# Optimization experiments

Hardware: AMD Instinct MI355X
Metric: run time of the kernel (lower is better)

Reference implementation:

```python
import jax, jax.numpy as jnp
import numpy as np

T, H, I, E, K = 16384, 2048, 1024, 8, 2  # tokens, hidden, intermediate, experts, top_k


def setup_inputs() -> dict:
    key = jax.random.key(0)
    k1, k2, k3, k4, k5 = jax.random.split(key, 5)
    hidden_states = jax.random.normal(k1, (T, H), dtype=jnp.float32)
    expert_routing_table = jax.random.randint(k2, (T, K), 0, E, dtype=jnp.int32)
    rw = jax.random.uniform(k3, (T, K), dtype=jnp.float32)
    router_weights = rw  # op consumes raw per-token gate weights
    # fused gate+up projection per expert: [E, 2I, H] (Linear-style [out, in])
    w13 = jax.random.normal(k4, (E, 2 * I, H), dtype=jnp.float32) * (1.0 / np.sqrt(H))
    # down projection per expert: [E, H, I]
    w2 = jax.random.normal(k5, (E, H, I), dtype=jnp.float32) * (1.0 / np.sqrt(I))
    return {
        "hidden_states": hidden_states,
        "expert_routing_table": expert_routing_table,
        "router_weights": router_weights,
        "w13": w13,
        "w2": w2,
    }


def reference(hidden_states, expert_routing_table, router_weights, w13, w2):
    # Faithful math of torch.ops.hpu.mixture_of_experts (silu activation):
    # for each token t and each routed expert e (top-k):
    #   g, u = split(x_t @ w13_e^T); y += router_w * ((silu(g) * u) @ w2_e^T)
    num_experts = w13.shape[0]
    out = jnp.zeros_like(hidden_states)
    for e in range(num_experts):  # small fixed expert loop
        # combine weight for expert e per token: sum over top-k slots routed to e
        coef = jnp.sum(
            jnp.where(expert_routing_table == e, router_weights, 0.0), axis=-1
        )  # [T]
        gu = hidden_states @ w13[e].T            # [T, 2I]
        g, u = jnp.split(gu, 2, axis=-1)         # SwiGLU halves
        act = jax.nn.silu(g) * u                 # [T, I]
        out = out + coef[:, None] * (act @ w2[e].T)  # [T, H]
    return out
```

## Files before the change

kernel.cpp:

```cpp
#include <hip/hip_runtime.h>
#include <hip/hip_bf16.h>
#include <stdint.h>

#define TOKS 16384
#define HDIM 2048
#define IDIM 1024
#define NEXP 8
#define TOPK 2
#define NPAIR (TOKS*TOPK)

typedef __attribute__((ext_vector_type(4))) float f32x4;
typedef __attribute__((ext_vector_type(8))) __bf16 bf16x8;
typedef __attribute__((ext_vector_type(8))) unsigned short u16x8;

#define GLOAD_LDS16(gp, lp) \
  __builtin_amdgcn_global_load_lds((const __attribute__((address_space(1))) void*)(gp), \
                                   (__attribute__((address_space(3))) void*)(lp), 16, 0, 0)

#define LGKM_WAITN(n) asm volatile("s_waitcnt lgkmcnt(" #n ")" ::: "memory")
#define VM_WAITN(n)   asm volatile("s_waitcnt vmcnt(" #n ")" ::: "memory")

__device__ __forceinline__ unsigned short f2bf(float f) {
  unsigned int u = __float_as_uint(f);
  u += 0x7FFF + ((u >> 16) & 1);
  return (unsigned short)(u >> 16);
}
__device__ __forceinline__ float bf2f(unsigned short h) {
  return __uint_as_float(((unsigned int)h) << 16);
}

#define W13_N8 (NEXP * 2 * IDIM * HDIM / 8)
#define W2_N8  (NEXP * HDIM * IDIM / 8)
#define X_N8   (TOKS * HDIM / 8)
__global__ __launch_bounds__(256) void cvt_all(const float* __restrict__ w13,
                                               const float* __restrict__ w2,
                                               const float* __restrict__ x,
                                               unsigned short* __restrict__ w13b,
                                               unsigned short* __restrict__ w2b,
                                               unsigned short* __restrict__ xb) {
  int i = blockIdx.x * 256 + threadIdx.x;
  const float* s; unsigned short* d; int j;
  if (i < W13_N8)              { s = w13; d = w13b; j = i; }
  else if (i < W13_N8 + W2_N8) { s = w2;  d = w2b;  j = i - W13_N8; }
  else                         { s = x;   d = xb;   j = i - W13_N8 - W2_N8; }
  const float4* sp = (const float4*)s + (size_t)j * 2;
  float4 a = sp[0], b = sp[1];
  u16x8 o;
  o[0] = f2bf(a.x); o[1] = f2bf(a.y); o[2] = f2bf(a.z); o[3] = f2bf(a.w);
  o[4] = f2bf(b.x); o[5] = f2bf(b.y); o[6] = f2bf(b.z); o[7] = f2bf(b.w);
  *((u16x8*)d + j) = o;
}

__global__ void route_count(const int* __restrict__ ert, int* __restrict__ ctrl) {
  int p = blockIdx.x * 256 + threadIdx.x;
  if (p < NPAIR) atomicAdd(&ctrl[ert[p]], 1);
}

__global__ void route_scan(int* __restrict__ ctrl) {
  if (blockIdx.x == 0 && threadIdx.x == 0) {
    int off = 0;
    for (int e = 0; e < NEXP; ++e) { ctrl[8 + e] = off; ctrl[16 + e] = off; off += ctrl[e]; }
    int toff = 0;
    for (int e = 0; e < NEXP; ++e) { ctrl[24 + e] = toff; toff += (ctrl[e] + 255) >> 8; }
    ctrl[32] = toff;
  }
}

__global__ void route_scatter(const int* __restrict__ ert, const float* __restrict__ rw,
                              int* __restrict__ ctrl, int* __restrict__ porig,
                              float* __restrict__ pcoef, int* __restrict__ pinv) {
  int p = blockIdx.x * 256 + threadIdx.x;
  if (p < NPAIR) {
    int e = ert[p];
    int pos = atomicAdd(&ctrl[16 + e], 1);
    porig[pos] = p;
    pcoef[pos] = rw[p];
    pinv[p]    = pos;
  }
}


#define RD_SET(lb, A0v, A1v, B0v, B1v) do {                                          \
  _Pragma("unroll") for (int mi = 0; mi < 4; ++mi) {                                 \
    int r_ = wr * 128 + mi * 16 + l15;                                               \
    A0v[mi] = *(const bf16x8*)((lb) + r_ * 64 + ((l16 ^ ((r_ >> 1) & 3)) << 4)); }   \
  _Pragma("unroll") for (int ni = 0; ni < 2; ++ni) {                                 \
    int nb_ = wc * 64 + ni * 16 + l15;                                               \
    B0v[ni] = *(const bf16x8*)((lb) + 16384 + nb_ * 64 + ((l16 ^ ((nb_ >> 1) & 3)) << 4)); } \
  _Pragma("unroll") for (int ni = 0; ni < 2; ++ni) {                                 \
    int nb_ = wc * 64 + 32 + ni * 16 + l15;                                          \
    B1v[ni] = *(const bf16x8*)((lb) + 16384 + nb_ * 64 + ((l16 ^ ((nb_ >> 1) & 3)) << 4)); } \
  _Pragma("unroll") for (int mi = 0; mi < 4; ++mi) {                                 \
    int r_ = wr * 128 + 64 + mi * 16 + l15;                                          \
    A1v[mi] = *(const bf16x8*)((lb) + r_ * 64 + ((l16 ^ ((r_ >> 1) & 3)) << 4)); }   \
} while (0)

#define MMQ(qm, qn, Av, Bv) do {                                                     \
  _Pragma("unroll") for (int mi = 0; mi < 4; ++mi)                                   \
    _Pragma("unroll") for (int ni = 0; ni < 2; ++ni)                                 \
      acc[qm][qn][mi][ni] = __builtin_amdgcn_mfma_f32_16x16x32_bf16(                 \
          Av[mi], Bv[ni], acc[qm][qn][mi][ni], 0, 0, 0);                             \
} while (0)

#define ITER(i, cA0, cA1, cB0, cB1, nA0, nA1, nB0, nB1) do {                         \
  if ((i) + 3 < NT) STAGE((i) + 3);                                                  \
  LGKM_WAITN(6);                                                                     \
  __builtin_amdgcn_s_setprio(1); MMQ(0, 0, cA0, cB0);                                \
  LGKM_WAITN(4);                 MMQ(0, 1, cA0, cB1);                                \
  __builtin_amdgcn_s_setprio(0);                                                     \
  LGKM_WAITN(0);                                                                     \
  if ((i) < NT - 1) {                                                                \
    if ((i) + 3 < NT)       { VM_WAITN(8); }                                         \
    else if ((i) + 3 == NT) { VM_WAITN(4); }                                         \
    else                    { VM_WAITN(0); }                                         \
    __builtin_amdgcn_s_barrier();                                                    \
    RD_SET(lds + (((i) + 1) & 3) * 32768, nA0, nA1, nB0, nB1);                       \
    __builtin_amdgcn_sched_barrier(0);                                               \
  }                                                                                  \
  __builtin_amdgcn_s_setprio(1); MMQ(1, 0, cA1, cB0); MMQ(1, 1, cA1, cB1);           \
  __builtin_amdgcn_s_setprio(0);                                                     \
} while (0)

#define TILE_MAP()                                                                   \
  const int x_ = bid & 7, k_ = bid >> 3;                                             \
  const int cb = k_ & 7;                                                             \
  const int tile = ((k_ >> 3) << 3) + x_;

__global__ __launch_bounds__(512, 2) void gemm1(const unsigned short* __restrict__ xb,
                                                const unsigned short* __restrict__ w13b,
                                                const int* __restrict__ ctrl,
                                                const int* __restrict__ porig,
                                                unsigned short* __restrict__ actb) {
  __shared__ __align__(16) char lds[131072];
  const int bid  = blockIdx.x;
  TILE_MAP();
  if (tile >= ctrl[32]) return;
  int e = 7;
  #pragma unroll
  for (int k = 7; k >= 1; --k) if (tile < ctrl[24 + k]) e = k - 1;
  const int rb   = tile - ctrl[24 + e];
  const int Ne   = ctrl[e];
  const int base = ctrl[8 + e];
  const int row0 = rb * 256;
  const int c0   = cb * 128;
  const int tid  = threadIdx.x;
  const int wid  = tid >> 6;
  const int lane = tid & 63;
  const int wr   = wid >> 2;
  const int wc   = wid & 3;
  const int l15  = lane & 15;
  const int l16  = lane >> 4;
  const int NT   = HDIM / 32;

  const unsigned short *gA0, *gA1, *gB0, *gB1;
  {
    int rl = wid * 16 + (lane >> 2);
    int r0 = rl, r1 = 128 + rl;
    int c80 = (lane & 3) ^ ((r0 >> 1) & 3);
    int c81 = (lane & 3) ^ ((r1 >> 1) & 3);
    int rr0 = row0 + r0; if (rr0 > Ne - 1) rr0 = Ne - 1;
    int rr1 = row0 + r1; if (rr1 > Ne - 1) rr1 = Ne - 1;
    gA0 = xb + (size_t)(porig[base + rr0] >> 1) * HDIM + c80 * 8;
    gA1 = xb + (size_t)(porig[base + rr1] >> 1) * HDIM + c81 * 8;
    int g0 = ((r0 & 32) ? IDIM : 0) + c0 + ((r0 >> 6) << 5) + (r0 & 31);
    int g1 = ((r1 & 32) ? IDIM : 0) + c0 + ((r1 >> 6) << 5) + (r1 & 31);
    gB0 = w13b + ((size_t)e * (2 * IDIM) + g0) * HDIM + c80 * 8;
    gB1 = w13b + ((size_t)e * (2 * IDIM) + g1) * HDIM + c81 * 8;
  }

  f32x4 acc[2][2][4][2];
  #pragma unroll
  for (int qm = 0; qm < 2; ++qm)
    #pragma unroll
    for (int qn = 0; qn < 2; ++qn)
      #pragma unroll
      for (int mi = 0; mi < 4; ++mi)
        #pragma unroll
        for (int ni = 0; ni < 2; ++ni) acc[qm][qn][mi][ni] = (f32x4)(0.0f);

  auto STAGE = [&](int kt) {
    char* d = lds + (kt & 3) * 32768 + wid * 1024;
    GLOAD_LDS16(gA0 + kt * 32, d);
    GLOAD_LDS16(gA1 + kt * 32, d + 8192);
    GLOAD_LDS16(gB0 + kt * 32, d + 16384);
    GLOAD_LDS16(gB1 + kt * 32, d + 24576);
  };

  bf16x8 A0a[4], A1a[4], B0a[2], B1a[2];
  bf16x8 A0b[4], A1b[4], B0b[2], B1b[2];

  STAGE(0); STAGE(1); STAGE(2);
  VM_WAITN(8);
  __builtin_amdgcn_s_barrier();
  RD_SET(lds, A0a, A1a, B0a, B1a);
  __builtin_amdgcn_sched_barrier(0);

  for (int i = 0; i < NT; i += 2) {
    ITER(i,     A0a, A1a, B0a, B1a, A0b, A1b, B0b, B1b);
    ITER(i + 1, A0b, A1b, B0b, B1b, A0a, A1a, B0a, B1a);
  }

  #pragma unroll
  for (int qm = 0; qm < 2; ++qm)
    #pragma unroll
    for (int mi = 0; mi < 4; ++mi)
      #pragma unroll
      for (int jj = 0; jj < 4; ++jj) {
        int r = wr * 128 + qm * 64 + mi * 16 + l16 * 4 + jj;
        int rr = row0 + r;
        if (rr < Ne) {
          #pragma unroll
          for (int ni = 0; ni < 2; ++ni) {
            float g = acc[qm][0][mi][ni][jj];
            float u = acc[qm][1][mi][ni][jj];
            float a = g / (1.0f + __expf(-g)) * u;
            actb[(size_t)(base + rr) * IDIM + (c0 + wc * 32 + ni * 16 + l15)] = f2bf(a);
          }
        }
      }
}

__global__ __launch_bounds__(512, 2) void gemm2(const unsigned short* __restrict__ actb,
                                                const unsigned short* __restrict__ w2b,
                                                const int* __restrict__ ctrl,
                                                const float* __restrict__ pcoef,
                                                unsigned short* __restrict__ yb) {
  __shared__ __align__(16) char lds[131072];
  const int bid  = blockIdx.x;
  TILE_MAP();
  if (tile >= ctrl[32]) return;
  int e = 7;
  #pragma unroll
  for (int k = 7; k >= 1; --k) if (tile < ctrl[24 + k]) e = k - 1;
  const int rb   = tile - ctrl[24 + e];
  const int Ne   = ctrl[e];
  const int base = ctrl[8 + e];
  const int row0 = rb * 256;
  const int n0   = cb * 256;
  const int tid  = threadIdx.x;
  const int wid  = tid >> 6;
  const int lane = tid & 63;
  const int wr   = wid >> 2;
  const int wc   = wid & 3;
  const int l15  = lane & 15;
  const int l16  = lane >> 4;
  const int NT   = IDIM / 32;

  const unsigned short *gA0, *gA1, *gB0, *gB1;
  {
    int rl = wid * 16 + (lane >> 2);
    int r0 = rl, r1 = 128 + rl;
    int c80 = (lane & 3) ^ ((r0 >> 1) & 3);
    int c81 = (lane & 3) ^ ((r1 >> 1) & 3);
    int rr0 = row0 + r0; if (rr0 > Ne - 1) rr0 = Ne - 1;
    int rr1 = row0 + r1; if (rr1 > Ne - 1) rr1 = Ne - 1;
    gA0 = actb + (size_t)(base + rr0) * IDIM + c80 * 8;
    gA1 = actb + (size_t)(base + rr1) * IDIM + c81 * 8;
    gB0 = w2b + ((size_t)e * HDIM + n0 + r0) * IDIM + c80 * 8;
    gB1 = w2b + ((size_t)e * HDIM + n0 + r1) * IDIM + c81 * 8;
  }

  f32x4 acc[2][2][4][2];
  #pragma unroll
  for (int qm = 0; qm < 2; ++qm)
    #pragma unroll
    for (int qn = 0; qn < 2; ++qn)
      #pragma unroll
      for (int mi = 0; mi < 4; ++mi)
        #pragma unroll
        for (int ni = 0; ni < 2; ++ni) acc[qm][qn][mi][ni] = (f32x4)(0.0f);

  auto STAGE = [&](int kt) {
    char* d = lds + (kt & 3) * 32768 + wid * 1024;
    GLOAD_LDS16(gA0 + kt * 32, d);
    GLOAD_LDS16(gA1 + kt * 32, d + 8192);
    GLOAD_LDS16(gB0 + kt * 32, d + 16384);
    GLOAD_LDS16(gB1 + kt * 32, d + 24576);
  };

  bf16x8 A0a[4], A1a[4], B0a[2], B1a[2];
  bf16x8 A0b[4], A1b[4], B0b[2], B1b[2];

  STAGE(0); STAGE(1); STAGE(2);
  VM_WAITN(8);
  __builtin_amdgcn_s_barrier();
  RD_SET(lds, A0a, A1a, B0a, B1a);
  __builtin_amdgcn_sched_barrier(0);

  for (int i = 0; i < NT; i += 2) {
    ITER(i,     A0a, A1a, B0a, B1a, A0b, A1b, B0b, B1b);
    ITER(i + 1, A0b, A1b, B0b, B1b, A0a, A1a, B0a, B1a);
  }

  #pragma unroll
  for (int qm = 0; qm < 2; ++qm)
    #pragma unroll
    for (int mi = 0; mi < 4; ++mi)
      #pragma unroll
      for (int jj = 0; jj < 4; ++jj) {
        int r = wr * 128 + qm * 64 + mi * 16 + l16 * 4 + jj;
        int rr = row0 + r;
        if (rr < Ne) {
          float cf = pcoef[base + rr];
          #pragma unroll
          for (int qn = 0; qn < 2; ++qn)
            #pragma unroll
            for (int ni = 0; ni < 2; ++ni) {
              int col = n0 + wc * 64 + qn * 32 + ni * 16 + l15;
              yb[(size_t)(base + rr) * HDIM + col] = f2bf(acc[qm][qn][mi][ni][jj] * cf);
            }
        }
      }
}

__global__ __launch_bounds__(256) void reduce2(const unsigned short* __restrict__ yb,
                                               const int* __restrict__ pinv,
                                               float* __restrict__ out) {
  int i = blockIdx.x * 256 + threadIdx.x;
  int t = i >> 8;
  int g = i & 255;
  int p0 = pinv[2 * t], p1 = pinv[2 * t + 1];
  u16x8 a = *((const u16x8*)(yb + (size_t)p0 * HDIM) + g);
  u16x8 b = *((const u16x8*)(yb + (size_t)p1 * HDIM) + g);
  float4 o0, o1;
  o0.x = bf2f(a[0]) + bf2f(b[0]); o0.y = bf2f(a[1]) + bf2f(b[1]);
  o0.z = bf2f(a[2]) + bf2f(b[2]); o0.w = bf2f(a[3]) + bf2f(b[3]);
  o1.x = bf2f(a[4]) + bf2f(b[4]); o1.y = bf2f(a[5]) + bf2f(b[5]);
  o1.z = bf2f(a[6]) + bf2f(b[6]); o1.w = bf2f(a[7]) + bf2f(b[7]);
  float4* dst = (float4*)(out + (size_t)t * HDIM) + g * 2;
  dst[0] = o0; dst[1] = o1;
}

extern "C" void kernel_launch(void* const* d_in, const int* in_sizes, int n_in,
                              void* d_out, int out_size, void* d_ws, size_t ws_size,
                              hipStream_t stream) {
  const float* x   = (const float*)d_in[0];
  const int*   ert = (const int*)d_in[1];
  const float* rw  = (const float*)d_in[2];
  const float* w13 = (const float*)d_in[3];
  const float* w2  = (const float*)d_in[4];
  float* out = (float*)d_out;

  char* ws = (char*)d_ws;
  size_t off = 0;
  auto alloc = [&](size_t bytes) { char* p = ws + off; off += (bytes + 255) & ~255ULL; return p; };
  int*            ctrl  = (int*)           alloc(256);
  int*            porig = (int*)           alloc((size_t)NPAIR * 4);
  float*          pcoef = (float*)         alloc((size_t)NPAIR * 4);
  int*            pinv  = (int*)           alloc((size_t)NPAIR * 4);
  unsigned short* w2b   = (unsigned short*)alloc((size_t)NEXP * HDIM * IDIM * 2);
  unsigned short* actb  = (unsigned short*)alloc((size_t)NPAIR * IDIM * 2);
  unsigned short* w13b  = (unsigned short*)alloc((size_t)NEXP * 2 * IDIM * HDIM * 2);
  unsigned short* xb    = (unsigned short*)alloc((size_t)TOKS * HDIM * 2);
  unsigned short* yb    = w13b;

  hipMemsetAsync(ctrl, 0, 256, stream);

  cvt_all<<<(W13_N8 + W2_N8 + X_N8) / 256, 256, 0, stream>>>(w13, w2, x, w13b, w2b, xb);

  route_count  <<<NPAIR / 256, 256, 0, stream>>>(ert, ctrl);
  route_scan   <<<1, 64, 0, stream>>>(ert ? ctrl : ctrl);
  route_scatter<<<NPAIR / 256, 256, 0, stream>>>(ert, rw, ctrl, porig, pcoef, pinv);

  gemm1<<<136 * 8, 512, 0, stream>>>(xb, w13b, ctrl, porig, actb);
  gemm2<<<136 * 8, 512, 0, stream>>>(actb, w2b, ctrl, pcoef, yb);
  reduce2<<<(TOKS * HDIM / 8) / 256, 256, 0, stream>>>(yb, pinv, out);
}
```

Baseline: 821.8 us.

## Interleave next-tile LDS fragment reads between MFMA quadrants in GEMM main loop

Restructures the software-pipelined GEMM loop used by both expert GEMMs. The barrier and global-load wait now come at the start of each iteration, and the next tile's LDS fragment reads are split into three groups placed between the four MFMA quadrant blocks, instead of one bulk read after a mid-iteration barrier. This aims to hide LDS read latency behind matrix-core work and take the barrier off the middle of the compute sequence. The tighter waitcnt and sched_barrier choreography risks stalls or correctness problems if the counts do not match the outstanding operations.

New measurement: 861.4 us. 1.05x slower.

```diff
diff --git a/kernel.cpp b/kernel.cpp
--- a/kernel.cpp
+++ b/kernel.cpp
@@ -19,6 +19,7 @@
 
 #define LGKM_WAITN(n) asm volatile("s_waitcnt lgkmcnt(" #n ")" ::: "memory")
 #define VM_WAITN(n)   asm volatile("s_waitcnt vmcnt(" #n ")" ::: "memory")
+#define SBAR0()       __builtin_amdgcn_sched_barrier(0)
 
 __device__ __forceinline__ unsigned short f2bf(float f) {
   unsigned int u = __float_as_uint(f);
@@ -80,45 +81,53 @@
 }
 
 
-#define RD_SET(lb, A0v, A1v, B0v, B1v) do {                                          \
+#define RD_A0C(lb, A0v) do {                                                         \
   _Pragma("unroll") for (int mi = 0; mi < 4; ++mi) {                                 \
     int r_ = wr * 128 + mi * 16 + l15;                                               \
     A0v[mi] = *(const bf16x8*)((lb) + r_ * 64 + ((l16 ^ ((r_ >> 1) & 3)) << 4)); }   \
+} while (0)
+
+#define RD_BC(lb, B0v, B1v) do {                                                     \
   _Pragma("unroll") for (int ni = 0; ni < 2; ++ni) {                                 \
     int nb_ = wc * 64 + ni * 16 + l15;                                               \
     B0v[ni] = *(const bf16x8*)((lb) + 16384 + nb_ * 64 + ((l16 ^ ((nb_ >> 1) & 3)) << 4)); } \
   _Pragma("unroll") for (int ni = 0; ni < 2; ++ni) {                                 \
     int nb_ = wc * 64 + 32 + ni * 16 + l15;                                          \
     B1v[ni] = *(const bf16x8*)((lb) + 16384 + nb_ * 64 + ((l16 ^ ((nb_ >> 1) & 3)) << 4)); } \
+} while (0)
+
+#define RD_A1C(lb, A1v) do {                                                         \
   _Pragma("unroll") for (int mi = 0; mi < 4; ++mi) {                                 \
     int r_ = wr * 128 + 64 + mi * 16 + l15;                                          \
     A1v[mi] = *(const bf16x8*)((lb) + r_ * 64 + ((l16 ^ ((r_ >> 1) & 3)) << 4)); }   \
 } while (0)
 
 #define MMQ(qm, qn, Av, Bv) do {                                                     \
+  __builtin_amdgcn_s_setprio(1);                                                     \
   _Pragma("unroll") for (int mi = 0; mi < 4; ++mi)                                   \
     _Pragma("unroll") for (int ni = 0; ni < 2; ++ni)                                 \
       acc[qm][qn][mi][ni] = __builtin_amdgcn_mfma_f32_16x16x32_bf16(                 \
           Av[mi], Bv[ni], acc[qm][qn][mi][ni], 0, 0, 0);                             \
+  __builtin_amdgcn_s_setprio(0);                                                     \
 } while (0)
 
 #define ITER(i, cA0, cA1, cB0, cB1, nA0, nA1, nB0, nB1) do {                         \
-  if ((i) + 3 < NT) STAGE((i) + 3);                                                  \
-  LGKM_WAITN(6);                                                                     \
-  __builtin_amdgcn_s_setprio(1); MMQ(0, 0, cA0, cB0);                                \
-  LGKM_WAITN(4);                 MMQ(0, 1, cA0, cB1);                                \
-  __builtin_amdgcn_s_setprio(0);                                                     \
-  LGKM_WAITN(0);                                                                     \
-  if ((i) < NT - 1) {                                                                \
-    if ((i) + 3 < NT)       { VM_WAITN(8); }                                         \
-    else if ((i) + 3 == NT) { VM_WAITN(4); }                                         \
-    else                    { VM_WAITN(0); }                                         \
-    __builtin_amdgcn_s_barrier();                                                    \
-    RD_SET(lds + (((i) + 1) & 3) * 32768, nA0, nA1, nB0, nB1);                       \
-    __builtin_amdgcn_sched_barrier(0);                                               \
-  }                                                                                  \
-  __builtin_amdgcn_s_setprio(1); MMQ(1, 0, cA1, cB0); MMQ(1, 1, cA1, cB1);           \
-  __builtin_amdgcn_s_setprio(0);                                                     \
+  if ((i) < NT - 2) { VM_WAITN(4); } else { VM_WAITN(0); }                           \
+  __builtin_amdgcn_s_barrier();       \
+  if ((i) + 3 < NT) STAGE((i) + 3);                       \
+  const char* lbn_ = lds + (((i) + 1) & 3) * 32768;                                  \
+  LGKM_WAITN(6); SBAR0();                                                            \
+  MMQ(0, 0, cA0, cB0);                                                               \
+  if ((i) < NT - 1) { RD_A0C(lbn_, nA0); SBAR0(); LGKM_WAITN(8); }                   \
+  else              { LGKM_WAITN(4); }                                               \
+  SBAR0();                                                                           \
+  MMQ(0, 1, cA0, cB1);                                                               \
+  if ((i) < NT - 1) { RD_BC(lbn_, nB0, nB1); SBAR0(); LGKM_WAITN(8); }               \
+  else              { LGKM_WAITN(0); }                                               \
+  SBAR0();                                                                           \
+  MMQ(1, 0, cA1, cB0);                                                               \
+  if ((i) < NT - 1) { RD_A1C(lbn_, nA1); SBAR0(); }                                  \
+  MMQ(1, 1, cA1, cB1);                                                               \
 } while (0)
 
 #define TILE_MAP()                                                                   \
@@ -192,8 +201,8 @@
   STAGE(0); STAGE(1); STAGE(2);
   VM_WAITN(8);
   __builtin_amdgcn_s_barrier();
-  RD_SET(lds, A0a, A1a, B0a, B1a);
-  __builtin_amdgcn_sched_barrier(0);
+  RD_A0C(lds, A0a); RD_BC(lds, B0a, B1a); RD_A1C(lds, A1a);
+  SBAR0();
 
   for (int i = 0; i < NT; i += 2) {
     ITER(i,     A0a, A1a, B0a, B1a, A0b, A1b, B0b, B1b);
@@ -284,8 +293,8 @@
   STAGE(0); STAGE(1); STAGE(2);
   VM_WAITN(8);
   __builtin_amdgcn_s_barrier();
-  RD_SET(lds, A0a, A1a, B0a, B1a);
-  __builtin_amdgcn_sched_barrier(0);
+  RD_A0C(lds, A0a); RD_BC(lds, B0a, B1a); RD_A1C(lds, A1a);
+  SBAR0();
 
   for (int i = 0; i < NT; i += 2) {
     ITER(i,     A0a, A1a, B0a, B1a, A0b, A1b, B0b, B1b);
@@ -359,7 +368,7 @@
   cvt_all<<<(W13_N8 + W2_N8 + X_N8) / 256, 256, 0, stream>>>(w13, w2, x, w13b, w2b, xb);
 
   route_count  <<<NPAIR / 256, 256, 0, stream>>>(ert, ctrl);
-  route_scan   <<<1, 64, 0, stream>>>(ert ? ctrl : ctrl);
+  route_scan   <<<1, 64, 0, stream>>>(ctrl);
   route_scatter<<<NPAIR / 256, 256, 0, stream>>>(ert, rw, ctrl, porig, pcoef, pinv);
 
   gemm1<<<136 * 8, 512, 0, stream>>>(xb, w13b, ctrl, porig, actb);
```
